# Optimization experiments

Hardware: AMD Instinct MI355X
Metric: run time of the kernel (lower is better)

Reference implementation:

```python
import jax, jax.numpy as jnp
import numpy as np

N = 8192          # number of prototypes
D = 128           # proto_dim == hidden_dim (residual requires equality)
H = 2             # GAT heads
K = 3             # k_neighbors + 1 (k_neighbors=2 hard-coded in forward)
NEG_SLOPE = 0.2   # PyG GATConv default leaky relu slope
LN_EPS = 1e-5


def setup_inputs() -> dict:
    key = jax.random.key(0)
    ks = jax.random.split(key, 6)
    prototypes = jax.random.normal(ks[0], (N, D), dtype=jnp.float32)
    labels = jax.random.randint(ks[1], (N,), 0, 1024, dtype=jnp.int64)
    # GATConv params: lin maps D -> H*D (concat=False => per-head dim = hidden_dim)
    W = jax.random.normal(ks[2], (D, H * D), dtype=jnp.float32) / np.sqrt(D)
    att_src = jax.random.normal(ks[3], (H, D), dtype=jnp.float32) / np.sqrt(D)
    att_dst = jax.random.normal(ks[4], (H, D), dtype=jnp.float32) / np.sqrt(D)
    bias = jnp.zeros((D,), dtype=jnp.float32)
    gamma = jnp.ones((D,), dtype=jnp.float32)   # LayerNorm weight
    beta = jnp.zeros((D,), dtype=jnp.float32)   # LayerNorm bias
    return {"prototypes": prototypes, "labels": labels, "W": W,
            "att_src": att_src, "att_dst": att_dst, "bias": bias,
            "gamma": gamma, "beta": beta}


def _knn_edges(x):
    # Squared euclidean distances (same ordering as torch.cdist -> same topk indices).
    sq = jnp.sum(x * x, axis=-1)
    d2 = sq[:, None] + sq[None, :] - 2.0 * (x @ x.T)          # [N, N]
    _, idx = jax.lax.top_k(-d2, K)                            # [N, K] smallest dists
    # topk includes self (dist 0); module masks self-edges then GATConv re-adds
    # self loops, so the effective edge set is exactly the topk set -> static E=N*K.
    src = jnp.repeat(jnp.arange(x.shape[0]), K)               # edge source j
    dst = idx.reshape(-1)                                     # edge target i
    return src, dst


def _gat(x, src, dst, W, att_src, att_dst, bias):
    n = x.shape[0]
    xp = (x @ W).reshape(n, H, D)                             # [N, H, C]
    a_s = jnp.sum(xp * att_src[None], axis=-1)                # [N, H]
    a_d = jnp.sum(xp * att_dst[None], axis=-1)                # [N, H]
    e = a_s[src] + a_d[dst]                                   # [E, H]
    e = jax.nn.leaky_relu(e, NEG_SLOPE)
    # segment softmax over incoming edges of each destination node
    m = jax.ops.segment_max(e, dst, num_segments=n)           # [N, H]
    w = jnp.exp(e - m[dst])
    denom = jax.ops.segment_sum(w, dst, num_segments=n)       # [N, H]
    alpha = w / denom[dst]                                    # [E, H]
    msg = alpha[:, :, None] * xp[src]                         # [E, H, C]
    out = jax.ops.segment_sum(msg, dst, num_segments=n)       # [N, H, C]
    return out.mean(axis=1) + bias                            # concat=False -> head mean


def reference(prototypes, labels, W, att_src, att_dst, bias, gamma, beta):
    x = prototypes
    src, dst = _knn_edges(x)
    x_new = _gat(x, src, dst, W, att_src, att_dst, bias)
    mu = jnp.mean(x_new, axis=-1, keepdims=True)
    var = jnp.var(x_new, axis=-1, keepdims=True)
    x_new = (x_new - mu) * jax.lax.rsqrt(var + LN_EPS) * gamma + beta
    x_new = jax.nn.relu(x_new)
    # dropout layers are identity in eval mode
    return x + x_new
```

## Files before the change

### kernel.cpp

```cpp
#include <hip/hip_runtime.h>
#include <hip/hip_bf16.h>
#include <math.h>

#define GN 8192
#define GD 128
#define GH 2
#define GK 3
#define NEG_SLOPE 0.2f
#define LN_EPS 1e-5f

using short8  = __attribute__((ext_vector_type(8)))  short;
using float16 = __attribute__((ext_vector_type(16))) float;
using f32x4   = __attribute__((ext_vector_type(4)))  float;

__device__ __forceinline__ float wred(float v) {
    #pragma unroll
    for (int o = 32; o > 0; o >>= 1) v += __shfl_xor(v, o, 64);
    return v;
}

__device__ __forceinline__ unsigned fenc(float f) {
    unsigned b = __float_as_uint(f);
    return (b & 0x80000000u) ? ~b : (b | 0x80000000u);
}

__device__ __forceinline__ float rawbf2f(unsigned short s) {
    return __uint_as_float(((unsigned)s) << 16);
}
__device__ __forceinline__ unsigned short f2rawbf(float f) {
    __hip_bfloat16 b = __float2bfloat16(f);
    unsigned short r; __builtin_memcpy(&r, &b, 2);
    return r;
}
__device__ __forceinline__ unsigned umin2(unsigned a, unsigned b) { return a < b ? a : b; }
__device__ __forceinline__ unsigned umax2(unsigned a, unsigned b) { return a > b ? a : b; }

__global__ void k_pre(const float* __restrict__ W, const float* __restrict__ att_src,
                      const float* __restrict__ att_dst,
                      unsigned short* __restrict__ Wth, unsigned short* __restrict__ Wtl,
                      float* __restrict__ uvec) {
    __shared__ float vs[128];
    int b = blockIdx.x, t = threadIdx.x;
    if (b < 128) {
        int e = b * 256 + t;
        int d = e >> 8, j = e & 255;
        int h = j >> 7, c = j & 127;
        int k = h * 128 + d;
        float w = W[e];
        unsigned short hi = f2rawbf(w);
        Wth[c * 256 + k] = hi;
        Wtl[c * 256 + k] = f2rawbf(w - rawbf2f(hi));
    } else {
        int bb = b - 128;
        int h = bb & 1;
        const float* v = (bb < 2 ? att_src : att_dst) + h * 128;
        if (t < 128) vs[t] = v[t];
        __syncthreads();
        int d = t >> 1, half = t & 1;
        const float* wr = W + (size_t)d * 256 + h * 128 + half * 64;
        float s = 0.f;
        for (int c = 0; c < 64; c++) s += wr[c] * vs[half * 64 + c];
        s += __shfl_xor(s, 1, 64);
        if (half == 0) uvec[bb * 128 + d] = s;
    }
}

__global__ void k_conv(const float* __restrict__ x, const float* __restrict__ uvec,
                       float* __restrict__ sq,
                       unsigned short* __restrict__ xa, unsigned short* __restrict__ xb,
                       float* __restrict__ a_s, float* __restrict__ a_d,
                       int* __restrict__ cnt, int* __restrict__ curs) {
    int row = blockIdx.x * 4 + (threadIdx.x >> 6);
    int lane = threadIdx.x & 63;
    const float* xr = x + (size_t)row * GD;
    float a0 = xr[lane], a1 = xr[lane + 64];
    float s = wred(a0 * a0 + a1 * a1);
    unsigned short* ar = xa + (size_t)row * 144;
    unsigned short* br = xb + (size_t)row * 144;
    ar[lane] = f2rawbf(-2.f * a0); ar[lane + 64] = f2rawbf(-2.f * a1);
    br[lane] = f2rawbf(a0);        br[lane + 64] = f2rawbf(a1);
    float s0 = wred(a0 * uvec[lane]       + a1 * uvec[64 + lane]);
    float s1 = wred(a0 * uvec[128 + lane] + a1 * uvec[192 + lane]);
    float d0 = wred(a0 * uvec[256 + lane] + a1 * uvec[320 + lane]);
    float d1 = wred(a0 * uvec[384 + lane] + a1 * uvec[448 + lane]);
    if (lane < 16) {
        unsigned short av = 0, bv = 0;
        if (lane == 0)      { av = f2rawbf(s + 512.f); bv = 0x3F80; }
        else if (lane == 1) { float hi = rawbf2f(f2rawbf(s + 512.f));
                              av = f2rawbf(s + 512.f - hi); bv = 0x3F80; }
        ar[128 + lane] = av; br[128 + lane] = bv;
        if (lane == 0) {
            sq[row] = s;
            a_s[row * 2] = s0; a_s[row * 2 + 1] = s1;
            a_d[row * 2] = d0; a_d[row * 2 + 1] = d1;
            cnt[row] = 0; curs[row] = 0;
        }
    }
}

__launch_bounds__(256, 4)
__global__ void k_gemm_topk(const unsigned short* __restrict__ xa,
                            const unsigned short* __restrict__ xb,
                            unsigned* __restrict__ cand) {
    __shared__ unsigned short At[18 * 128 * 8];
    int t = threadIdx.x;
    int w = t >> 6, lane = t & 63, h = lane >> 5, n = lane & 31;
    int col = blockIdx.x * 128 + w * 32 + n;
    int sb = blockIdx.y;

    short8 bfrag[9];
    #pragma unroll
    for (int kc = 0; kc < 9; kc++)
        bfrag[kc] = *(const short8*)(xb + (size_t)col * 144 + (2 * kc + h) * 8);

    unsigned T0 = 0xFFFFFFFFu, T1 = 0xFFFFFFFFu, T2 = 0xFFFFFFFFu, T3 = 0xFFFFFFFFu;

    for (int it = 0; it < 4; it++) {
        int rowbase = sb * 512 + it * 128;
        __syncthreads();
        #pragma unroll
        for (int s = 0; s < 9; s++) {
            int q = t + 256 * s;
            int kb = q >> 7, r = q & 127;
            __builtin_amdgcn_global_load_lds(
                (const __attribute__((address_space(1))) unsigned*)
                    (xa + (size_t)(rowbase + r) * 144 + kb * 8),
                (__attribute__((address_space(3))) unsigned*)&At[q * 8],
                16, 0, 0);
        }
        __syncthreads();

        float16 acc[4];
        #pragma unroll
        for (int rs = 0; rs < 4; rs++) acc[rs] = (float16)(0.f);

        #pragma unroll
        for (int kc = 0; kc < 9; kc++) {
            short8 a[4];
            #pragma unroll
            for (int rs = 0; rs < 4; rs++)
                a[rs] = *(const short8*)&At[((2 * kc + h) * 128 + rs * 32 + n) * 8];
            #pragma unroll
            for (int rs = 0; rs < 4; rs++)
                acc[rs] = __builtin_amdgcn_mfma_f32_32x32x16_bf16(a[rs], bfrag[kc], acc[rs], 0, 0, 0);
        }

        #pragma unroll
        for (int rs = 0; rs < 4; rs++) {
            float16 A = acc[rs];
            unsigned b[16];
            #pragma unroll
            for (int r = 0; r < 16; r++) b[r] = __float_as_uint(A[r]);
            unsigned ma = umin2(umin2(umin2(b[0],b[1]),umin2(b[2],b[3])),
                                umin2(umin2(b[4],b[5]),umin2(b[6],b[7])));
            unsigned mb = umin2(umin2(umin2(b[8],b[9]),umin2(b[10],b[11])),
                                umin2(umin2(b[12],b[13]),umin2(b[14],b[15])));
            if ((umin2(ma, mb) & 0xFFFFE000u) <= T3) {
                int rb = rowbase + 4 * h + rs * 32;
                #pragma unroll
                for (int r = 0; r < 16; r++) {
                    unsigned k = (b[r] & 0xFFFFE000u) |
                                 (unsigned)(rb + (r & 3) + 8 * (r >> 2));
                    unsigned m0 = umax2(T0, k);  T0 = umin2(T0, k);
                    unsigned m1 = umax2(T1, m0); T1 = umin2(T1, m0);
                    unsigned m2 = umax2(T2, m1); T2 = umin2(T2, m1);
                    T3 = umin2(T3, m2);
                }
            }
        }
    }

    unsigned p0 = (unsigned)__shfl_xor((int)T0, 32), p1 = (unsigned)__shfl_xor((int)T1, 32),
             p2 = (unsigned)__shfl_xor((int)T2, 32), p3 = (unsigned)__shfl_xor((int)T3, 32);
    #pragma unroll
    for (int q = 0; q < 4; q++) {
        unsigned k = (q == 0) ? p0 : (q == 1) ? p1 : (q == 2) ? p2 : p3;
        unsigned m0 = umax2(T0, k);  T0 = umin2(T0, k);
        unsigned m1 = umax2(T1, m0); T1 = umin2(T1, m0);
        unsigned m2 = umax2(T2, m1); T2 = umin2(T2, m1);
        T3 = umin2(T3, m2);
    }

    if (h == 0) {
        uint4 o = make_uint4(T0, T1, T2, T3);
        *(uint4*)(cand + (size_t)col * 64 + sb * 4) = o;
    }
}

__device__ __forceinline__ int clampN(int v) {
    return v < 0 ? 0 : (v >= GN ? GN - 1 : v);
}

__global__ void k_refine(const unsigned* __restrict__ cand,
                         const float* __restrict__ x, const float* __restrict__ sq,
                         int* __restrict__ fidx, int* __restrict__ cnt) {
    int t = threadIdx.x, wv = t >> 6, lane = t & 63;
    int j = blockIdx.x * 4 + wv;
    int c = lane >> 2, g = lane & 3;

    unsigned key32 = cand[(size_t)j * 64 + lane];
    int myidx = 0;
    #pragma unroll
    for (int r = 0; r < 16; r++) {
        unsigned m = key32;
        #pragma unroll
        for (int o = 32; o > 0; o >>= 1)
            m = umin2(m, (unsigned)__shfl_xor((int)m, o, 64));
        myidx = (c == r) ? (int)(m & 8191u) : myidx;
        key32 = (key32 == m) ? 0xFFFFFFFFu : key32;
    }

    const float* xi = x + (size_t)myidx * GD + g * 32;
    const float* xj = x + (size_t)j * GD + g * 32;
    float p = 0.f;
    #pragma unroll
    for (int d4 = 0; d4 < 8; d4++) {
        float4 a = *(const float4*)(xi + d4 * 4);
        float4 b = *(const float4*)(xj + d4 * 4);
        p += a.x * b.x + a.y * b.y + a.z * b.z + a.w * b.w;
    }
    p += __shfl_xor(p, 1, 64);
    p += __shfl_xor(p, 2, 64);
    float d2 = sq[j] + sq[myidx] - 2.f * p;
    unsigned long long key = ((unsigned long long)fenc(d2) << 32) | (unsigned)myidx;

    int out3[3];
    #pragma unroll
    for (int r = 0; r < 3; r++) {
        unsigned long long k = key;
        #pragma unroll
        for (int o = 4; o <= 32; o <<= 1) {
            unsigned long long other = __shfl_xor(k, o, 64);
            k = k < other ? k : other;
        }
        out3[r] = (int)(unsigned)(k & 8191u);
        key = (key == k) ? ~0ull : key;
    }
    if (lane == 0) {
        int i0 = clampN(out3[0]), i1 = clampN(out3[1]), i2 = clampN(out3[2]);
        fidx[j * 3 + 0] = i0; fidx[j * 3 + 1] = i1; fidx[j * 3 + 2] = i2;
        atomicAdd(&cnt[i0], 1); atomicAdd(&cnt[i1], 1); atomicAdd(&cnt[i2], 1);
    }
}

__global__ void k_scan(const int* __restrict__ cnt, int* __restrict__ offs) {
    __shared__ int part[256];
    int t = threadIdx.x;
    int base = t * 32;
    int loc[32];
    int s = 0;
    #pragma unroll
    for (int k = 0; k < 32; k++) { loc[k] = s; s += cnt[base + k]; }
    part[t] = s;
    __syncthreads();
    if (t == 0) {
        int run = 0;
        for (int k = 0; k < 256; k++) { int v = part[k]; part[k] = run; run += v; }
        offs[GN] = run;
    }
    __syncthreads();
    int b = part[t];
    #pragma unroll
    for (int k = 0; k < 32; k++) offs[base + k] = b + loc[k];
}

__global__ void k_fill(const int* __restrict__ fidx, const int* __restrict__ offs,
                       int* __restrict__ cursor, int* __restrict__ elist,
                       const float* __restrict__ a_s, const float* __restrict__ a_d,
                       float2* __restrict__ ew) {
    int eid = blockIdx.x * 256 + threadIdx.x;
    int i = clampN(fidx[eid]);
    int src = eid / 3;
    float2 as = ((const float2*)a_s)[src];
    float2 ad = ((const float2*)a_d)[i];
    float e0 = as.x + ad.x; e0 = e0 >= 0.f ? e0 : NEG_SLOPE * e0;
    float e1 = as.y + ad.y; e1 = e1 >= 0.f ? e1 : NEG_SLOPE * e1;
    float w0 = expf(e0), w1 = expf(e1);
    int pos = atomicAdd(&cursor[i], 1);
    int slot = offs[i] + pos;
    if (slot < GN * GK) { elist[slot] = src; ew[slot] = make_float2(w0, w1); }
}

__launch_bounds__(512, 4)
__global__ void k_out(const int* __restrict__ offs, const int* __restrict__ elst,
                      const float2* __restrict__ ew,
                      const float* __restrict__ x,
                      const unsigned short* __restrict__ Wth,
                      const unsigned short* __restrict__ Wtl,
                      const float* __restrict__ bias, const float* __restrict__ gamma,
                      const float* __restrict__ beta, float* __restrict__ out) {
    __shared__ unsigned short zh[16][264];
    __shared__ unsigned short zl[16][264];
    __shared__ float os[16][132];
    int t = threadIdx.x, i0 = blockIdx.x * 16;
    int wv = t >> 6, lane = t & 63;
    int eslot = lane >> 3, g = lane & 7;

    #pragma unroll
    for (int pp = 0; pp < 2; pp++) {
        int r = wv * 2 + pp, node = i0 + r;
        int s = offs[node], e = offs[node + 1];
        float acc0[16], acc1[16];
        #pragma unroll
        for (int q = 0; q < 16; q++) { acc0[q] = 0.f; acc1[q] = 0.f; }
        float w0s = 0.f, w1s = 0.f;
        for (int k0 = s; k0 < e; k0 += 8) {
            int k = k0 + eslot;
            bool valid = k < e;
            int j = valid ? elst[k] : 0;
            float2 wv2 = valid ? ew[k] : make_float2(0.f, 0.f);
            const float* xr = x + (size_t)j * GD + g * 16;
            float4 x0 = *(const float4*)(xr);
            float4 x1 = *(const float4*)(xr + 4);
            float4 x2 = *(const float4*)(xr + 8);
            float4 x3 = *(const float4*)(xr + 12);
            float xv[16] = {x0.x, x0.y, x0.z, x0.w, x1.x, x1.y, x1.z, x1.w,
                            x2.x, x2.y, x2.z, x2.w, x3.x, x3.y, x3.z, x3.w};
            #pragma unroll
            for (int q = 0; q < 16; q++) {
                acc0[q] += wv2.x * xv[q];
                acc1[q] += wv2.y * xv[q];
            }
            w0s += wv2.x; w1s += wv2.y;
        }
        #pragma unroll
        for (int m = 8; m <= 32; m <<= 1) {
            #pragma unroll
            for (int q = 0; q < 16; q++) {
                acc0[q] += __shfl_xor(acc0[q], m, 64);
                acc1[q] += __shfl_xor(acc1[q], m, 64);
            }
            w0s += __shfl_xor(w0s, m, 64);
            w1s += __shfl_xor(w1s, m, 64);
        }
        if (lane < 8) {
            float dn0 = 0.5f / w0s, dn1 = 0.5f / w1s;
            #pragma unroll
            for (int q = 0; q < 16; q += 2) {
                float a0 = acc0[q] * dn0, a1 = acc0[q + 1] * dn0;
                unsigned short h0 = f2rawbf(a0), h1 = f2rawbf(a1);
                *(unsigned*)&zh[r][lane * 16 + q] = (unsigned)h0 | ((unsigned)h1 << 16);
                *(unsigned*)&zl[r][lane * 16 + q] =
                    (unsigned)f2rawbf(a0 - rawbf2f(h0)) |
                    ((unsigned)f2rawbf(a1 - rawbf2f(h1)) << 16);
                float b0 = acc1[q] * dn1, b1 = acc1[q + 1] * dn1;
                unsigned short p0 = f2rawbf(b0), p1 = f2rawbf(b1);
                *(unsigned*)&zh[r][128 + lane * 16 + q] = (unsigned)p0 | ((unsigned)p1 << 16);
                *(unsigned*)&zl[r][128 + lane * 16 + q] =
                    (unsigned)f2rawbf(b0 - rawbf2f(p0)) |
                    ((unsigned)f2rawbf(b1 - rawbf2f(p1)) << 16);
            }
        }
    }
    __syncthreads();

    {
        int qd = lane >> 4, an = lane & 15;
        int c = wv * 16 + an;
        f32x4 acc = {0.f, 0.f, 0.f, 0.f};
        #pragma unroll
        for (int s = 0; s < 8; s++) {
            int ko = s * 32 + qd * 8;
            short8 ah = *(const short8*)&zh[an][ko];
            short8 al = *(const short8*)&zl[an][ko];
            short8 bh = *(const short8*)(Wth + (size_t)c * 256 + ko);
            short8 bl = *(const short8*)(Wtl + (size_t)c * 256 + ko);
            acc = __builtin_amdgcn_mfma_f32_16x16x32_bf16(ah, bh, acc, 0, 0, 0);
            acc = __builtin_amdgcn_mfma_f32_16x16x32_bf16(al, bh, acc, 0, 0, 0);
            acc = __builtin_amdgcn_mfma_f32_16x16x32_bf16(ah, bl, acc, 0, 0, 0);
        }
        #pragma unroll
        for (int r = 0; r < 4; r++) os[qd * 4 + r][c] = acc[r];
    }
    __syncthreads();

    #pragma unroll
    for (int pp = 0; pp < 2; pp++) {
        int r = wv * 2 + pp, node = i0 + r;
        float y0 = os[r][lane] + bias[lane];
        float y1 = os[r][lane + 64] + bias[lane + 64];
        float mu = wred(y0 + y1) * (1.f / 128.f);
        float c0 = y0 - mu, c1 = y1 - mu;
        float var = wred(c0 * c0 + c1 * c1) * (1.f / 128.f);
        float rs2 = 1.f / sqrtf(var + LN_EPS);
        float n0 = c0 * rs2 * gamma[lane] + beta[lane];
        float n1 = c1 * rs2 * gamma[lane + 64] + beta[lane + 64];
        n0 = n0 > 0.f ? n0 : 0.f;
        n1 = n1 > 0.f ? n1 : 0.f;
        out[(size_t)node * GD + lane]      = x[(size_t)node * GD + lane] + n0;
        out[(size_t)node * GD + lane + 64] = x[(size_t)node * GD + lane + 64] + n1;
    }
}

extern "C" void kernel_launch(void* const* d_in, const int* in_sizes, int n_in,
                              void* d_out, int out_size, void* d_ws, size_t ws_size,
                              hipStream_t stream) {
    const float* x       = (const float*)d_in[0];
    const float* W       = (const float*)d_in[2];
    const float* att_src = (const float*)d_in[3];
    const float* att_dst = (const float*)d_in[4];
    const float* bias    = (const float*)d_in[5];
    const float* gamma   = (const float*)d_in[6];
    const float* beta    = (const float*)d_in[7];
    float* out = (float*)d_out;

    char* w = (char*)d_ws;
    unsigned short* xa = (unsigned short*)w; w += (size_t)GN * 144 * 2;
    unsigned short* xb = (unsigned short*)w; w += (size_t)GN * 144 * 2;
    unsigned* cand = (unsigned*)w;           w += (size_t)GN * 64 * 4;
    float2* ew  = (float2*)w; w += (size_t)GN * GK * 8;
    unsigned short* Wth = (unsigned short*)w; w += (size_t)256 * 128 * 2;
    unsigned short* Wtl = (unsigned short*)w; w += (size_t)256 * 128 * 2;
    float* uvec = (float*)w; w += (size_t)4 * 128 * 4;
    float* sq   = (float*)w; w += (size_t)GN * 4;
    float* a_s  = (float*)w; w += (size_t)GN * GH * 4;
    float* a_d  = (float*)w; w += (size_t)GN * GH * 4;
    int*   fidx = (int*)w;   w += (size_t)GN * GK * 4;
    int*   cnt  = (int*)w;   w += (size_t)GN * 4;
    int*   curs = (int*)w;   w += (size_t)GN * 4;
    int*   offs = (int*)w;   w += (size_t)(GN + 1) * 4;
    int*   elst = (int*)w;   w += (size_t)GN * GK * 4;
    size_t need = (size_t)((char*)w - (char*)d_ws);
    if (ws_size < need) return;

    k_pre<<<132, 256, 0, stream>>>(W, att_src, att_dst, Wth, Wtl, uvec);
    k_conv<<<GN / 4, 256, 0, stream>>>(x, uvec, sq, xa, xb, a_s, a_d, cnt, curs);
    k_gemm_topk<<<dim3(64, 16), 256, 0, stream>>>(xa, xb, cand);
    k_refine<<<GN / 4, 256, 0, stream>>>(cand, x, sq, fidx, cnt);
    k_scan<<<1, 256, 0, stream>>>(cnt, offs);
    k_fill<<<GN * GK / 256, 256, 0, stream>>>(fidx, offs, curs, elst, a_s, a_d, ew);
    k_out<<<GN / 16, 512, 0, stream>>>(offs, elst, ew, x, Wth, Wtl, bias, gamma, beta, out);
}
```

Baseline: 174.7 us.

## Double-buffer LDS tiles in GEMM-topk and process two row segments per block

Adds a second LDS buffer so the next 128-row tile of xa is loaded with global_load_lds while MFMAs run on the current tile. Each block now covers two 512-row segments, which halves the grid and amortizes the B-fragment loads. Launch bounds drop from 4 to 2 blocks per CU because LDS use doubles. The risk is lower occupancy and fewer blocks (512) to spread across the CUs.

```diff
diff --git a/kernel.cpp b/kernel.cpp
--- a/kernel.cpp
+++ b/kernel.cpp
@@ -98,92 +98,110 @@
     }
 }
 
-__launch_bounds__(256, 4)
+#define STAGE_TILE(buf, rowbase)                                                  \
+    do {                                                                          \
+        _Pragma("unroll")                                                         \
+        for (int s_ = 0; s_ < 9; s_++) {                                          \
+            int q_ = t + 256 * s_;                                                \
+            int kb_ = q_ >> 7, r_ = q_ & 127;                                     \
+            __builtin_amdgcn_global_load_lds(                                     \
+                (const __attribute__((address_space(1))) unsigned*)               \
+                    (xa + (size_t)((rowbase) + r_) * 144 + kb_ * 8),              \
+                (__attribute__((address_space(3))) unsigned*)&At[(buf)][q_ * 8],  \
+                16, 0, 0);                                                        \
+        }                                                                         \
+    } while (0)
+
+__launch_bounds__(256, 2)
 __global__ void k_gemm_topk(const unsigned short* __restrict__ xa,
                             const unsigned short* __restrict__ xb,
                             unsigned* __restrict__ cand) {
-    __shared__ unsigned short At[18 * 128 * 8];
+    __shared__ unsigned short At[2][18 * 128 * 8];
     int t = threadIdx.x;
     int w = t >> 6, lane = t & 63, h = lane >> 5, n = lane & 31;
     int col = blockIdx.x * 128 + w * 32 + n;
-    int sb = blockIdx.y;
+    int sb0 = blockIdx.y * 2;
+    int rb0 = sb0 * 512;
 
     short8 bfrag[9];
     #pragma unroll
     for (int kc = 0; kc < 9; kc++)
         bfrag[kc] = *(const short8*)(xb + (size_t)col * 144 + (2 * kc + h) * 8);
 
-    unsigned T0 = 0xFFFFFFFFu, T1 = 0xFFFFFFFFu, T2 = 0xFFFFFFFFu, T3 = 0xFFFFFFFFu;
-
-    for (int it = 0; it < 4; it++) {
-        int rowbase = sb * 512 + it * 128;
-        __syncthreads();
-        #pragma unroll
-        for (int s = 0; s < 9; s++) {
-            int q = t + 256 * s;
-            int kb = q >> 7, r = q & 127;
-            __builtin_amdgcn_global_load_lds(
-                (const __attribute__((address_space(1))) unsigned*)
-                    (xa + (size_t)(rowbase + r) * 144 + kb * 8),
-                (__attribute__((address_space(3))) unsigned*)&At[q * 8],
-                16, 0, 0);
-        }
-        __syncthreads();
-
-        float16 acc[4];
-        #pragma unroll
-        for (int rs = 0; rs < 4; rs++) acc[rs] = (float16)(0.f);
-
-        #pragma unroll
-        for (int kc = 0; kc < 9; kc++) {
-            short8 a[4];
-            #pragma unroll
-            for (int rs = 0; rs < 4; rs++)
-                a[rs] = *(const short8*)&At[((2 * kc + h) * 128 + rs * 32 + n) * 8];
-            #pragma unroll
-            for (int rs = 0; rs < 4; rs++)
-                acc[rs] = __builtin_amdgcn_mfma_f32_32x32x16_bf16(a[rs], bfrag[kc], acc[rs], 0, 0, 0);
-        }
-
-        #pragma unroll
-        for (int rs = 0; rs < 4; rs++) {
-            float16 A = acc[rs];
-            unsigned b[16];
-            #pragma unroll
-            for (int r = 0; r < 16; r++) b[r] = __float_as_uint(A[r]);
-            unsigned ma = umin2(umin2(umin2(b[0],b[1]),umin2(b[2],b[3])),
-                                umin2(umin2(b[4],b[5]),umin2(b[6],b[7])));
-            unsigned mb = umin2(umin2(umin2(b[8],b[9]),umin2(b[10],b[11])),
-                                umin2(umin2(b[12],b[13]),umin2(b[14],b[15])));
-            if ((umin2(ma, mb) & 0xFFFFE000u) <= T3) {
-                int rb = rowbase + 4 * h + rs * 32;
+    STAGE_TILE(0, rb0);
+    asm volatile("s_waitcnt vmcnt(0)" ::: "memory");
+    __builtin_amdgcn_s_barrier();
+
+    #pragma unroll 1
+    for (int ss = 0; ss < 2; ss++) {
+        unsigned T0 = 0xFFFFFFFFu, T1 = 0xFFFFFFFFu, T2 = 0xFFFFFFFFu, T3 = 0xFFFFFFFFu;
+
+        #pragma unroll 1
+        for (int it = 0; it < 4; it++) {
+            int idx = ss * 4 + it;
+            int cur = idx & 1;
+            if (idx < 7) STAGE_TILE(cur ^ 1, rb0 + (idx + 1) * 128);
+
+            float16 acc[4];
+            #pragma unroll
+            for (int rs = 0; rs < 4; rs++) acc[rs] = (float16)(0.f);
+
+            #pragma unroll
+            for (int kc = 0; kc < 9; kc++) {
+                short8 a[4];
                 #pragma unroll
-                for (int r = 0; r < 16; r++) {
-                    unsigned k = (b[r] & 0xFFFFE000u) |
-                                 (unsigned)(rb + (r & 3) + 8 * (r >> 2));
-                    unsigned m0 = umax2(T0, k);  T0 = umin2(T0, k);
-                    unsigned m1 = umax2(T1, m0); T1 = umin2(T1, m0);
-                    unsigned m2 = umax2(T2, m1); T2 = umin2(T2, m1);
-                    T3 = umin2(T3, m2);
+                for (int rs = 0; rs < 4; rs++)
+                    a[rs] = *(const short8*)&At[cur][((2 * kc + h) * 128 + rs * 32 + n) * 8];
+                #pragma unroll
+                for (int rs = 0; rs < 4; rs++)
+                    acc[rs] = __builtin_amdgcn_mfma_f32_32x32x16_bf16(a[rs], bfrag[kc], acc[rs], 0, 0, 0);
+            }
+
+            int rowbase = rb0 + idx * 128;
+            #pragma unroll
+            for (int rs = 0; rs < 4; rs++) {
+                float16 A = acc[rs];
+                unsigned b[16];
+                #pragma unroll
+                for (int r = 0; r < 16; r++) b[r] = __float_as_uint(A[r]);
+                unsigned ma = umin2(umin2(umin2(b[0],b[1]),umin2(b[2],b[3])),
+                                    umin2(umin2(b[4],b[5]),umin2(b[6],b[7])));
+                unsigned mb = umin2(umin2(umin2(b[8],b[9]),umin2(b[10],b[11])),
+                                    umin2(umin2(b[12],b[13]),umin2(b[14],b[15])));
+                if ((umin2(ma, mb) & 0xFFFFE000u) <= T3) {
+                    int rb = rowbase + 4 * h + rs * 32;
+                    #pragma unroll
+                    for (int r = 0; r < 16; r++) {
+                        unsigned k = (b[r] & 0xFFFFE000u) |
+                                     (unsigned)(rb + (r & 3) + 8 * (r >> 2));
+                        unsigned m0 = umax2(T0, k);  T0 = umin2(T0, k);
+                        unsigned m1 = umax2(T1, m0); T1 = umin2(T1, m0);
+                        unsigned m2 = umax2(T2, m1); T2 = umin2(T2, m1);
+                        T3 = umin2(T3, m2);
+                    }
                 }
             }
-        }
-    }
-
-    unsigned p0 = (unsigned)__shfl_xor((int)T0, 32), p1 = (unsigned)__shfl_xor((int)T1, 32),
-             p2 = (unsigned)__shfl_xor((int)T2, 32), p3 = (unsigned)__shfl_xor((int)T3, 32);
-    #pragma unroll
-    for (int q = 0; q < 4; q++) {
-        unsigned k = (q == 0) ? p0 : (q == 1) ? p1 : (q == 2) ? p2 : p3;
-        unsigned m0 = umax2(T0, k);  T0 = umin2(T0, k);
-        unsigned m1 = umax2(T1, m0); T1 = umin2(T1, m0);
-        unsigned m2 = umax2(T2, m1); T2 = umin2(T2, m1);
-        T3 = umin2(T3, m2);
-    }
-
-    if (h == 0) {
-        uint4 o = make_uint4(T0, T1, T2, T3);
-        *(uint4*)(cand + (size_t)col * 64 + sb * 4) = o;
+
+            if (idx < 7) {
+                asm volatile("s_waitcnt vmcnt(0)" ::: "memory");
+                __builtin_amdgcn_s_barrier();
+            }
+        }
+
+        unsigned p0 = (unsigned)__shfl_xor((int)T0, 32), p1 = (unsigned)__shfl_xor((int)T1, 32),
+                 p2 = (unsigned)__shfl_xor((int)T2, 32), p3 = (unsigned)__shfl_xor((int)T3, 32);
+        #pragma unroll
+        for (int q = 0; q < 4; q++) {
+            unsigned k = (q == 0) ? p0 : (q == 1) ? p1 : (q == 2) ? p2 : p3;
+            unsigned m0 = umax2(T0, k);  T0 = umin2(T0, k);
+            unsigned m1 = umax2(T1, m0); T1 = umin2(T1, m0);
+            unsigned m2 = umax2(T2, m1); T2 = umin2(T2, m1);
+            T3 = umin2(T3, m2);
+        }
+        if (h == 0) {
+            uint4 o = make_uint4(T0, T1, T2, T3);
+            *(uint4*)(cand + (size_t)col * 64 + (sb0 + ss) * 4) = o;
+        }
     }
 }
 
@@ -425,7 +443,7 @@
 
     k_pre<<<132, 256, 0, stream>>>(W, att_src, att_dst, Wth, Wtl, uvec);
     k_conv<<<GN / 4, 256, 0, stream>>>(x, uvec, sq, xa, xb, a_s, a_d, cnt, curs);
-    k_gemm_topk<<<dim3(64, 16), 256, 0, stream>>>(xa, xb, cand);
+    k_gemm_topk<<<dim3(64, 8), 256, 0, stream>>>(xa, xb, cand);
     k_refine<<<GN / 4, 256, 0, stream>>>(cand, x, sq, fidx, cnt);
     k_scan<<<1, 256, 0, stream>>>(cnt, offs);
     k_fill<<<GN * GK / 256, 256, 0, stream>>>(fidx, offs, curs, elst, a_s, a_d, ew);
```

Result: no change. 172.1 us (-1.5%).

## Double-buffer A tile in LDS to overlap global loads with MFMA top-k

Applied to the files above, without the earlier changes.

Splits each 128-row A tile into 64-row halves held in two LDS buffers and prefetches the next half with global_load_lds while the current half feeds the MFMAs and the top-k update. Only one barrier per step is needed instead of two, and load latency is meant to hide behind compute. In exchange there are twice as many loop iterations, each doing half the MFMA work per LDS load, and the explicit vmcnt waits may serialise anyway. LDS use stays about the same, so occupancy should not change.

```diff
diff --git a/kernel.cpp b/kernel.cpp
--- a/kernel.cpp
+++ b/kernel.cpp
@@ -98,55 +98,64 @@
     }
 }
 
+#define STAGE_HALF(buf, rowbase)                                                  \
+    do {                                                                          \
+        _Pragma("unroll")                                                         \
+        for (int s_ = 0; s_ < 5; s_++) {                                          \
+            if (s_ < 4 || t < 128) {                                              \
+                int q_ = s_ * 256 + t;           \
+                int kb_ = q_ >> 6, r_ = q_ & 63;                                  \
+                __builtin_amdgcn_global_load_lds(                                 \
+                    (const __attribute__((address_space(1))) unsigned*)           \
+                        (xa + (size_t)((rowbase) + r_) * 144 + kb_ * 8),          \
+                    (__attribute__((address_space(3))) unsigned*)&At[(buf)][q_ * 8],\
+                    16, 0, 0);                                                    \
+            }                                                                     \
+        }                                                                         \
+    } while (0)
+
 __launch_bounds__(256, 4)
 __global__ void k_gemm_topk(const unsigned short* __restrict__ xa,
                             const unsigned short* __restrict__ xb,
                             unsigned* __restrict__ cand) {
-    __shared__ unsigned short At[18 * 128 * 8];
+    __shared__ unsigned short At[2][18 * 64 * 8];
     int t = threadIdx.x;
     int w = t >> 6, lane = t & 63, h = lane >> 5, n = lane & 31;
     int col = blockIdx.x * 128 + w * 32 + n;
     int sb = blockIdx.y;
+    int rb0 = sb * 512;
 
     short8 bfrag[9];
     #pragma unroll
     for (int kc = 0; kc < 9; kc++)
         bfrag[kc] = *(const short8*)(xb + (size_t)col * 144 + (2 * kc + h) * 8);
 
+    STAGE_HALF(0, rb0);
+    asm volatile("s_waitcnt vmcnt(0)" ::: "memory");
+    __builtin_amdgcn_s_barrier();
+
     unsigned T0 = 0xFFFFFFFFu, T1 = 0xFFFFFFFFu, T2 = 0xFFFFFFFFu, T3 = 0xFFFFFFFFu;
 
-    for (int it = 0; it < 4; it++) {
-        int rowbase = sb * 512 + it * 128;
-        __syncthreads();
-        #pragma unroll
-        for (int s = 0; s < 9; s++) {
-            int q = t + 256 * s;
-            int kb = q >> 7, r = q & 127;
-            __builtin_amdgcn_global_load_lds(
-                (const __attribute__((address_space(1))) unsigned*)
-                    (xa + (size_t)(rowbase + r) * 144 + kb * 8),
-                (__attribute__((address_space(3))) unsigned*)&At[q * 8],
-                16, 0, 0);
-        }
-        __syncthreads();
-
-        float16 acc[4];
-        #pragma unroll
-        for (int rs = 0; rs < 4; rs++) acc[rs] = (float16)(0.f);
+    #pragma unroll 1
+    for (int ht = 0; ht < 8; ht++) {
+        int cur = ht & 1;
+        if (ht < 7) STAGE_HALF(cur ^ 1, rb0 + (ht + 1) * 64);
+
+        float16 acc[2];
+        #pragma unroll
+        for (int rs = 0; rs < 2; rs++) acc[rs] = (float16)(0.f);
 
         #pragma unroll
         for (int kc = 0; kc < 9; kc++) {
-            short8 a[4];
-            #pragma unroll
-            for (int rs = 0; rs < 4; rs++)
-                a[rs] = *(const short8*)&At[((2 * kc + h) * 128 + rs * 32 + n) * 8];
-            #pragma unroll
-            for (int rs = 0; rs < 4; rs++)
-                acc[rs] = __builtin_amdgcn_mfma_f32_32x32x16_bf16(a[rs], bfrag[kc], acc[rs], 0, 0, 0);
-        }
-
-        #pragma unroll
-        for (int rs = 0; rs < 4; rs++) {
+            short8 a0 = *(const short8*)&At[cur][(((2 * kc + h) * 64) + n) * 8];
+            short8 a1 = *(const short8*)&At[cur][(((2 * kc + h) * 64) + 32 + n) * 8];
+            acc[0] = __builtin_amdgcn_mfma_f32_32x32x16_bf16(a0, bfrag[kc], acc[0], 0, 0, 0);
+            acc[1] = __builtin_amdgcn_mfma_f32_32x32x16_bf16(a1, bfrag[kc], acc[1], 0, 0, 0);
+        }
+
+        int rowbase = rb0 + ht * 64;
+        #pragma unroll
+        for (int rs = 0; rs < 2; rs++) {
             float16 A = acc[rs];
             unsigned b[16];
             #pragma unroll
@@ -168,6 +177,11 @@
                 }
             }
         }
+
+        if (ht < 7) {
+            asm volatile("s_waitcnt vmcnt(0)" ::: "memory");
+            __builtin_amdgcn_s_barrier();
+        }
     }
 
     unsigned p0 = (unsigned)__shfl_xor((int)T0, 32), p1 = (unsigned)__shfl_xor((int)T1, 32),
@@ -180,7 +194,6 @@
         unsigned m2 = umax2(T2, m1); T2 = umin2(T2, m1);
         T3 = umin2(T3, m2);
     }
-
     if (h == 0) {
         uint4 o = make_uint4(T0, T1, T2, T3);
         *(uint4*)(cand + (size_t)col * 64 + sb * 4) = o;
```

Result: faster. 167.3 us (-4.2%).
